# Optimization experiments

Hardware: AMD Instinct MI355X
Metric: run time of the kernel (lower is better)

## Reference

```python
import jax, jax.numpy as jnp
import numpy as np

N_AGT, N_CTX, E, D = 100000, 150000, 500000, 128
EPS = 1e-5


def gn(x, g, b):
    # GroupNorm(1, C) on [N, C] == per-row layernorm over channels
    mu = jnp.mean(x, axis=-1, keepdims=True)
    var = jnp.mean((x - mu) ** 2, axis=-1, keepdims=True)
    return (x - mu) * jax.lax.rsqrt(var + EPS) * g + b


def setup_inputs() -> dict:
    key = jax.random.key(0)
    ks = jax.random.split(key, 24)
    def w(k, i, o):
        return jax.random.normal(k, (i, o), jnp.float32) * (1.0 / np.sqrt(i))
    inp = {
        "agts": jax.random.normal(ks[0], (N_AGT, D), jnp.float32),
        "ctx": jax.random.normal(ks[1], (N_CTX, D), jnp.float32),
        "agt_ctrs": jax.random.normal(ks[2], (N_AGT, 2), jnp.float32),
        "ctx_ctrs": jax.random.normal(ks[3], (N_CTX, 2), jnp.float32),
        # dist MLP: Linear(2,128,bias) -> ReLU -> Linear(128,128,no bias) -> GN -> ReLU
        "W_dist1": w(ks[4], 2, D), "b_dist1": jnp.zeros((D,), jnp.float32),
        "W_dist2": w(ks[5], D, D), "g_dist": jnp.ones((D,), jnp.float32), "b_dist": jnp.zeros((D,), jnp.float32),
        # query: Linear(128,128,no bias) -> GN -> ReLU
        "W_q": w(ks[6], D, D), "g_q": jnp.ones((D,), jnp.float32), "b_q": jnp.zeros((D,), jnp.float32),
        # ctx MLP: Linear(384,128,no bias)->GN->ReLU -> Linear(128,128,no bias)
        "W_c1": w(ks[7], 3 * D, D), "g_c1": jnp.ones((D,), jnp.float32), "b_c1": jnp.zeros((D,), jnp.float32),
        "W_c2": w(ks[8], D, D),
        # agt: Linear(128,128,no bias)
        "W_agt": w(ks[9], D, D),
        # norm after scatter
        "g_n": jnp.ones((D,), jnp.float32), "b_n": jnp.zeros((D,), jnp.float32),
        # linear: Linear(128,128,no bias)->GN (no act)
        "W_lin": w(ks[10], D, D), "g_lin": jnp.ones((D,), jnp.float32), "b_lin": jnp.zeros((D,), jnp.float32),
        # precomputed edge lists (dist<=100 mask in the original)
        "hi": jax.random.randint(ks[11], (E,), 0, N_AGT, jnp.int32),
        "wi": jax.random.randint(ks[12], (E,), 0, N_CTX, jnp.int32),
    }
    return inp


def reference(agts, ctx, agt_ctrs, ctx_ctrs,
              W_dist1, b_dist1, W_dist2, g_dist, b_dist,
              W_q, g_q, b_q,
              W_c1, g_c1, b_c1, W_c2,
              W_agt, g_n, b_n,
              W_lin, g_lin, b_lin,
              hi, wi):
    res = agts
    # gather + dist MLP
    d = agt_ctrs[hi] - ctx_ctrs[wi]                    # [E, 2]
    d = jax.nn.relu(d @ W_dist1 + b_dist1)             # [E, D]
    d = jax.nn.relu(gn(d @ W_dist2, g_dist, b_dist))
    # query from gathered agent features
    q = jax.nn.relu(gn(agts[hi] @ W_q, g_q, b_q))      # [E, D]
    # context message MLP
    c = jnp.concatenate([d, q, ctx[wi]], axis=1)       # [E, 3D]
    c = jax.nn.relu(gn(c @ W_c1, g_c1, b_c1))
    c = c @ W_c2                                       # [E, D]
    # scatter back, norm, residual
    a = agts @ W_agt                                   # [N_agt, D]
    a = a.at[hi].add(c)
    a = jax.nn.relu(gn(a, g_n, b_n))
    a = gn(a @ W_lin, g_lin, b_lin)
    a = jax.nn.relu(a + res)
    return a
```

## Files before the change

kernel.cpp:

```cpp
#include <hip/hip_runtime.h>
#include <math.h>

#define DD 128
#define CAP 32
constexpr float EPS = 1e-5f;

typedef __bf16 bf16x8 __attribute__((ext_vector_type(8)));
typedef float  f32x4  __attribute__((ext_vector_type(4)));

__device__ __forceinline__ float4 ld4(const float* p){ return *(const float4*)p; }

__device__ __forceinline__ bf16x8 cvt8(const float* p){
  bf16x8 r;
#pragma unroll
  for (int i=0;i<8;i++) r[i] = (__bf16)p[i];
  return r;
}

__global__ __launch_bounds__(256)
void pack_w(const float* W0, const float* W1, const float* W2, const float* W3,
            const float* W4, const float* W5, const float* W6, const float* W7,
            __bf16* dst){
  int gidx = blockIdx.x*256 + threadIdx.x;
  int mat  = gidx >> 11;
  int i    = gidx & 2047;
  int lane = i & 63, frag = i >> 6;
  int tn = frag >> 2, ks = frag & 3;
  int n  = tn*16 + (lane & 15);
  int k0 = ks*32 + (lane >> 4)*8;
  const float* W;
  switch(mat){
    case 0: W=W0; break; case 1: W=W1; break; case 2: W=W2; break; case 3: W=W3; break;
    case 4: W=W4; break; case 5: W=W5; break; case 6: W=W6; break; default: W=W7; break;
  }
  __bf16* d = dst + (size_t)mat*16384 + (size_t)i*8;
#pragma unroll
  for (int j=0;j<8;j++) d[j] = (__bf16)W[(size_t)(k0+j)*DD + n];
}

template<bool RELU>
__device__ __forceinline__ void gn_frag(f32x4 (&acc)[8], const float* __restrict__ g,
                                        const float* __restrict__ b, int m){
  float gv[8], bv[8];
#pragma unroll
  for (int t=0;t<8;t++){ gv[t]=g[t*16+m]; bv[t]=b[t*16+m]; }
#pragma unroll
  for (int r=0;r<4;r++){
    float s=0.f, sq=0.f;
#pragma unroll
    for (int t=0;t<8;t++){ float v=acc[t][r]; s+=v; sq=fmaf(v,v,sq); }
#pragma unroll
    for (int mk=1; mk<16; mk<<=1){ s+=__shfl_xor(s,mk,64); sq+=__shfl_xor(sq,mk,64); }
    float mu=s*(1.f/DD);
    float rs=rsqrtf(sq*(1.f/DD)-mu*mu+EPS);
#pragma unroll
    for (int t=0;t<8;t++){
      float v=(acc[t][r]-mu)*rs*gv[t]+bv[t];
      if (RELU) v=fmaxf(v,0.f);
      acc[t][r]=v;
    }
  }
}

__device__ __forceinline__ void mfma_lds(const bf16x8 (&af)[4], const __bf16* WL,
                                         f32x4 (&acc)[8], int lane){
#pragma unroll
  for (int tn=0;tn<8;tn++){
    f32x4 a; a[0]=0.f; a[1]=0.f; a[2]=0.f; a[3]=0.f;
#pragma unroll
    for (int ks=0;ks<4;ks++){
      bf16x8 bf = *(const bf16x8*)(WL + ((tn*4+ks)*64 + lane)*8);
      a = __builtin_amdgcn_mfma_f32_16x16x32_bf16(af[ks], bf, a, 0,0,0);
    }
    acc[tn]=a;
  }
}

__device__ __forceinline__ void stage_w(const __bf16* __restrict__ Wg, __bf16* WL, int w, int lane){
#pragma unroll
  for (int j=0;j<8;j++){
    int off = ((w*8+j)<<10) + lane*16;
    __builtin_amdgcn_global_load_lds(
      (const __attribute__((address_space(1))) void*)((const char*)Wg + off),
      (__attribute__((address_space(3))) void*)((char*)WL + ((w*8+j)<<10)),
      16, 0, 0);
  }
}

__device__ __forceinline__ void read_af(const __bf16* T, bf16x8 (&af)[4], int w, int lane){
  int m=lane&15, q=lane>>4;
#pragma unroll
  for (int ks=0;ks<4;ks++)
    af[ks] = *(const bf16x8*)(T + (16*w+m)*136 + ks*32 + q*8);
}

__device__ __forceinline__ void write_cfrag_bf16(__bf16* T, const f32x4 (&acc)[8], int w, int lane){
  int m=lane&15, q=lane>>4;
#pragma unroll
  for (int r=0;r<4;r++){
    int row=16*w+4*q+r;
#pragma unroll
    for (int t=0;t<8;t++) T[row*136 + t*16 + m] = (__bf16)acc[t][r];
  }
}

__device__ __forceinline__ void load_af_f32(const float* X, bf16x8 (&af)[4], int row, int M, int q){
  if (row < M){
    const float* xr = X + (size_t)row*DD;
#pragma unroll
    for (int ks=0;ks<4;ks++){
      float t[8];
      *(float4*)t     = ld4(xr + ks*32 + q*8);
      *(float4*)(t+4) = ld4(xr + ks*32 + q*8 + 4);
      af[ks] = cvt8(t);
    }
  } else {
#pragma unroll
    for (int ks=0;ks<4;ks++){
#pragma unroll
      for (int j=0;j<8;j++) af[ks][j]=(__bf16)0.f;
    }
  }
}

__global__ __launch_bounds__(256)
void prep_kernel(const int* __restrict__ hi, int E, int* __restrict__ counts, int* __restrict__ perm,
                 const float* __restrict__ agts,
                 const __bf16* __restrict__ Wp_q, const float* __restrict__ g_q, const float* __restrict__ b_q,
                 const __bf16* __restrict__ Wp_mid, const __bf16* __restrict__ Wp_agt,
                 __bf16* __restrict__ Aq2bf, float* __restrict__ baseF, int nA,
                 const float* __restrict__ ctx, const __bf16* __restrict__ Wp_chi,
                 __bf16* __restrict__ Ccbf, int nC,
                 int gBucket, int gA){
  __shared__ __bf16 T[64*136];
  __shared__ __bf16 WL[16384];
  int b = blockIdx.x;
  if (b < gBucket){
    int e = b*256 + threadIdx.x;
    if (e < E){
      int a = hi[e];
      int slot = atomicAdd(&counts[a], 1);
      if (slot < CAP) perm[(size_t)a*CAP + slot] = e;
    }
    return;
  }
  b -= gBucket;
  int tid=threadIdx.x, w=tid>>6, lane=tid&63, m=lane&15, q=lane>>4;
  if (b < gA){
    stage_w(Wp_q, WL, w, lane);
    int rowA = b*64 + 16*w + m;
    bf16x8 af_a[4];
    load_af_f32(agts, af_a, rowA, nA, q);
    f32x4 acc[8];
    __syncthreads();
    mfma_lds(af_a, WL, acc, lane);
    __syncthreads();
    stage_w(Wp_mid, WL, w, lane);
    gn_frag<true>(acc, g_q, b_q, m);
    write_cfrag_bf16(T, acc, w, lane);
    bf16x8 af_q[4];
    read_af(T, af_q, w, lane);
    __syncthreads();
    mfma_lds(af_q, WL, acc, lane);
#pragma unroll
    for (int r=0;r<4;r++){
      int row = b*64 + 16*w + 4*q + r;
      if (row < nA){
#pragma unroll
        for (int t=0;t<8;t++)
          Aq2bf[(size_t)row*DD + t*16 + m] = (__bf16)acc[t][r];
      }
    }
    if (baseF){
      __syncthreads();
      stage_w(Wp_agt, WL, w, lane);
      __syncthreads();
      mfma_lds(af_a, WL, acc, lane);
#pragma unroll
      for (int r=0;r<4;r++){
        int row = b*64 + 16*w + 4*q + r;
        if (row < nA){
#pragma unroll
          for (int t=0;t<8;t++)
            baseF[(size_t)row*DD + t*16 + m] = acc[t][r];
        }
      }
    }
  } else {
    int bid = b - gA;
    stage_w(Wp_chi, WL, w, lane);
    int rowA = bid*64 + 16*w + m;
    bf16x8 af[4];
    load_af_f32(ctx, af, rowA, nC, q);
    f32x4 acc[8];
    __syncthreads();
    mfma_lds(af, WL, acc, lane);
#pragma unroll
    for (int r=0;r<4;r++){
      int row = bid*64 + 16*w + 4*q + r;
      if (row < nC){
#pragma unroll
        for (int t=0;t<8;t++)
          Ccbf[(size_t)row*DD + t*16 + m] = (__bf16)acc[t][r];
      }
    }
  }
}

__global__ __launch_bounds__(256)
void edge_kernel(const float* __restrict__ agt_ctrs, const float* __restrict__ ctx_ctrs,
                 const int* __restrict__ hi, const int* __restrict__ wi,
                 const float* __restrict__ W1, const float* __restrict__ B1,
                 const __bf16* __restrict__ Wp_d2, const float* __restrict__ g_dist, const float* __restrict__ b_dist,
                 const __bf16* __restrict__ Wp_c1, const float* __restrict__ g_c1, const float* __restrict__ b_c1,
                 const __bf16* __restrict__ Wp_c2,
                 const __bf16* __restrict__ Aq2, const __bf16* __restrict__ Cc,
                 float* __restrict__ accOut, __bf16* __restrict__ edge_out, int E){
  __shared__ __bf16 T[64*136];
  __shared__ __bf16 WL[16384];
  int tid=threadIdx.x, w=tid>>6, lane=tid&63, m=lane&15, q=lane>>4;
  int eBase = blockIdx.x*64;
  int grow = tid>>2, gch = tid&3;
  int ge = eBase + grow;
  int ghe=0, gwe=0;
  if (ge < E){ ghe = hi[ge]; gwe = wi[ge]; }
  bf16x8 ga[4], gc[4];
  {
    const __bf16* ap = Aq2 + (size_t)ghe*DD + gch*32;
    const __bf16* cp = Cc  + (size_t)gwe*DD + gch*32;
#pragma unroll
    for (int c2=0;c2<4;c2++){ ga[c2]=*(const bf16x8*)(ap+c2*8); gc[c2]=*(const bf16x8*)(cp+c2*8); }
  }
  stage_w(Wp_d2, WL, w, lane);
  {
    int e0 = lane, e = eBase + e0;
    float dx=0.f, dy=0.f;
    if (e < E){
      int h0=hi[e], w0=wi[e];
      dx = agt_ctrs[2*h0]   - ctx_ctrs[2*w0];
      dy = agt_ctrs[2*h0+1] - ctx_ctrs[2*w0+1];
    }
#pragma unroll
    for (int s=0;s<4;s++){
      float t[8];
#pragma unroll
      for (int j=0;j<8;j++){
        int c = w*32 + s*8 + j;
        t[j] = fmaxf(fmaf(dx, W1[c], fmaf(dy, W1[DD+c], B1[c])), 0.f);
      }
      *(bf16x8*)(T + e0*136 + w*32 + s*8) = cvt8(t);
    }
  }
  __syncthreads();
  bf16x8 af[4]; f32x4 acc[8];
  read_af(T, af, w, lane);
  mfma_lds(af, WL, acc, lane);
  __syncthreads();
  stage_w(Wp_c1, WL, w, lane);
  gn_frag<true>(acc, g_dist, b_dist, m);
  write_cfrag_bf16(T, acc, w, lane);
  read_af(T, af, w, lane);
#pragma unroll
  for (int c2=0;c2<4;c2++){
    float s[8];
#pragma unroll
    for (int j=0;j<8;j++) s[j] = (float)ga[c2][j] + (float)gc[c2][j];
    *(bf16x8*)(T + grow*136 + gch*32 + c2*8) = cvt8(s);
  }
  __syncthreads();
  mfma_lds(af, WL, acc, lane);
#pragma unroll
  for (int r=0;r<4;r++){
    int row = 16*w + 4*q + r;
#pragma unroll
    for (int t=0;t<8;t++)
      acc[t][r] += (float)T[row*136 + t*16 + m];
  }
  __syncthreads();
  stage_w(Wp_c2, WL, w, lane);
  gn_frag<true>(acc, g_c1, b_c1, m);
  write_cfrag_bf16(T, acc, w, lane);
  read_af(T, af, w, lane);
  __syncthreads();
  mfma_lds(af, WL, acc, lane);
  if (edge_out){
    write_cfrag_bf16(T, acc, w, lane);
    if (ge < E){
      const __bf16* src = T + grow*136 + gch*32;
      __bf16* dst = edge_out + (size_t)ge*DD + gch*32;
#pragma unroll
      for (int c2=0;c2<4;c2++) *(bf16x8*)(dst + c2*8) = *(const bf16x8*)(src + c2*8);
    }
  } else {
#pragma unroll
    for (int r=0;r<4;r++){
      int row = 16*w + 4*q + r;
      if (eBase + row < E){
        int he = hi[eBase + row];
        float* dst = accOut + (size_t)he*DD + m;
#pragma unroll
        for (int t=0;t<8;t++)
          atomicAdd(dst + t*16, acc[t][r]);
      }
    }
  }
}

__global__ __launch_bounds__(256)
void final_fused(const float* __restrict__ agts, const __bf16* __restrict__ Wp_agt,
                 const int* __restrict__ counts, const int* __restrict__ perm,
                 const __bf16* __restrict__ edge_out,
                 const float* __restrict__ g_n, const float* __restrict__ b_n,
                 const __bf16* __restrict__ Wp_lin, const float* __restrict__ g_lin, const float* __restrict__ b_lin,
                 float* __restrict__ out, int M){
  __shared__ float Tf[64*132];
  __shared__ __bf16 T[64*136];
  __bf16* WA = (__bf16*)Tf;
  int tid=threadIdx.x, w=tid>>6, lane=tid&63, m=lane&15, q=lane>>4;
  int rowBase=blockIdx.x*64;
  stage_w(Wp_agt, WA, w, lane);
  bf16x8 af_a[4];
  load_af_f32(agts, af_a, rowBase + 16*w + m, M, q);
  f32x4 acc[8];
  __syncthreads();
  mfma_lds(af_a, WA, acc, lane);
  __syncthreads();
#pragma unroll
  for (int r=0;r<4;r++){
    int row=16*w+4*q+r;
#pragma unroll
    for (int t=0;t<8;t++) Tf[row*132 + t*16 + m] = acc[t][r];
  }
  int grow=tid>>2, gch=tid&3;
  int a = rowBase + grow;
  float s[32];
#pragma unroll
  for (int c2=0;c2<8;c2++){
    float4 v = *(const float4*)(Tf + grow*132 + gch*32 + c2*4);
    s[c2*4]=v.x; s[c2*4+1]=v.y; s[c2*4+2]=v.z; s[c2*4+3]=v.w;
  }
  __syncthreads();
  stage_w(Wp_lin, WA, w, lane);
  int cnt = 0;
  if (a < M){ cnt = counts[a]; cnt = cnt < CAP ? cnt : CAP; }
  for (int j=0;j<cnt;j++){
    int e = perm[(size_t)a*CAP + j];
    const __bf16* ep = edge_out + (size_t)e*DD + gch*32;
#pragma unroll
    for (int c2=0;c2<4;c2++){
      bf16x8 v = *(const bf16x8*)(ep + c2*8);
#pragma unroll
      for (int k=0;k<8;k++) s[c2*8+k] += (float)v[k];
    }
  }
  {
    float sm=0.f, sq=0.f;
#pragma unroll
    for (int k=0;k<32;k++){ sm+=s[k]; sq=fmaf(s[k],s[k],sq); }
    sm+=__shfl_xor(sm,1,64); sm+=__shfl_xor(sm,2,64);
    sq+=__shfl_xor(sq,1,64); sq+=__shfl_xor(sq,2,64);
    float mu=sm*(1.f/DD), rs=rsqrtf(sq*(1.f/DD)-mu*mu+EPS);
#pragma unroll
    for (int k=0;k<32;k++){
      int c=gch*32+k;
      s[k]=fmaxf((s[k]-mu)*rs*g_n[c]+b_n[c],0.f);
    }
  }
#pragma unroll
  for (int c2=0;c2<4;c2++)
    *(bf16x8*)(T + grow*136 + gch*32 + c2*8) = cvt8(s + c2*8);
  __syncthreads();
  bf16x8 af[4];
  read_af(T, af, w, lane);
  mfma_lds(af, WA, acc, lane);
  gn_frag<false>(acc, g_lin, b_lin, m);
#pragma unroll
  for (int r=0;r<4;r++){
    int row=rowBase+16*w+4*q+r;
    if (row<M){
#pragma unroll
      for (int t=0;t<8;t++){
        int col=t*16+m;
        float rr=agts[(size_t)row*DD+col];
        out[(size_t)row*DD+col]=fmaxf(acc[t][r]+rr,0.f);
      }
    }
  }
}

__global__ __launch_bounds__(256)
void final_kernel(const float* __restrict__ accF, const float* __restrict__ g_n, const float* __restrict__ b_n,
                  const __bf16* __restrict__ Wp_lin, const float* __restrict__ g_lin, const float* __restrict__ b_lin,
                  const float* __restrict__ res, float* __restrict__ out, int M){
  __shared__ __bf16 Ab[64*136];
  __shared__ __bf16 WL[16384];
  int tid=threadIdx.x, w=tid>>6, lane=tid&63, m=lane&15, q=lane>>4;
  int rowBase=blockIdx.x*64;
  stage_w(Wp_lin, WL, w, lane);
  {
    int rl=tid>>2, qq=tid&3;
    int row=rowBase+rl;
    float v[32];
    float s=0.f, sq=0.f;
#pragma unroll
    for (int t8=0;t8<8;t8++){
      float4 x=make_float4(0.f,0.f,0.f,0.f);
      if (row<M) x=ld4(accF + (size_t)row*DD + qq*32 + t8*4);
      v[t8*4]=x.x; v[t8*4+1]=x.y; v[t8*4+2]=x.z; v[t8*4+3]=x.w;
      s  += x.x+x.y+x.z+x.w;
      sq += x.x*x.x+x.y*x.y+x.z*x.z+x.w*x.w;
    }
    s+=__shfl_xor(s,1,64); s+=__shfl_xor(s,2,64);
    sq+=__shfl_xor(sq,1,64); sq+=__shfl_xor(sq,2,64);
    float mu=s*(1.f/DD), rs=rsqrtf(sq*(1.f/DD)-mu*mu+EPS);
#pragma unroll
    for (int j=0;j<32;j++){
      int c=qq*32+j;
      v[j]=fmaxf((v[j]-mu)*rs*g_n[c]+b_n[c],0.f);
    }
#pragma unroll
    for (int s2=0;s2<4;s2++)
      *(bf16x8*)(Ab + rl*136 + qq*32 + s2*8) = cvt8(v+s2*8);
  }
  __syncthreads();
  bf16x8 af[4]; f32x4 acc[8];
  read_af(Ab, af, w, lane);
  mfma_lds(af, WL, acc, lane);
  gn_frag<false>(acc, g_lin, b_lin, m);
#pragma unroll
  for (int r=0;r<4;r++){
    int row=rowBase+16*w+4*q+r;
    if (row<M){
#pragma unroll
      for (int t=0;t<8;t++){
        int col=t*16+m;
        float rr=res[(size_t)row*DD+col];
        out[(size_t)row*DD+col]=fmaxf(acc[t][r]+rr,0.f);
      }
    }
  }
}

extern "C" void kernel_launch(void* const* d_in, const int* in_sizes, int n_in,
                              void* d_out, int out_size, void* d_ws, size_t ws_size,
                              hipStream_t stream){
  const float* agts     = (const float*)d_in[0];
  const float* ctx      = (const float*)d_in[1];
  const float* agt_ctrs = (const float*)d_in[2];
  const float* ctx_ctrs = (const float*)d_in[3];
  const float* W_dist1  = (const float*)d_in[4];
  const float* b_dist1  = (const float*)d_in[5];
  const float* W_dist2  = (const float*)d_in[6];
  const float* g_dist   = (const float*)d_in[7];
  const float* b_dist   = (const float*)d_in[8];
  const float* W_q      = (const float*)d_in[9];
  const float* g_q      = (const float*)d_in[10];
  const float* b_q      = (const float*)d_in[11];
  const float* W_c1     = (const float*)d_in[12];
  const float* g_c1     = (const float*)d_in[13];
  const float* b_c1     = (const float*)d_in[14];
  const float* W_c2     = (const float*)d_in[15];
  const float* W_agt    = (const float*)d_in[16];
  const float* g_n      = (const float*)d_in[17];
  const float* b_n      = (const float*)d_in[18];
  const float* W_lin    = (const float*)d_in[19];
  const float* g_lin    = (const float*)d_in[20];
  const float* b_lin    = (const float*)d_in[21];
  const int*   hi       = (const int*)d_in[22];
  const int*   wi       = (const int*)d_in[23];

  int nA = in_sizes[0]/DD, nC = in_sizes[1]/DD, nE = in_sizes[22];
  float* out = (float*)d_out;

  auto al = [](size_t x){ return (x + 255) & ~(size_t)255; };
  size_t oAq2 = 0;
  size_t oCc  = al(oAq2 + (size_t)nA*DD*2);
  size_t oWp  = al(oCc  + (size_t)nC*DD*2);
  size_t oCnt = al(oWp  + (size_t)8*16384*2);
  size_t oPerm= al(oCnt + (size_t)nA*4);
  size_t oTail= al(oPerm+ (size_t)nA*CAP*4);
  size_t needA = oTail + (size_t)nE*DD*2;
  bool bigA = (ws_size >= needA);

  char* ws = (char*)d_ws;
  __bf16* Aq2bf = (__bf16*)(ws + oAq2);
  __bf16* Ccbf  = (__bf16*)(ws + oCc);
  __bf16* Wp    = (__bf16*)(ws + oWp);
  int*    counts= (int*)   (ws + oCnt);
  int*    perm  = (int*)   (ws + oPerm);
  __bf16* edge_out = (__bf16*)(ws + oTail);
  float*  CF    = (float*)(ws + oCnt);

  dim3 B(256);
  int gA=(nA+63)/64, gC=(nC+63)/64, gE=(nE+63)/64;
  int gBucket = bigA ? (nE+255)/256 : 0;

  pack_w<<<64,B,0,stream>>>(W_dist2, W_c1, W_c2, W_q,
                            W_c1+128*DD, W_c1+256*DD, W_agt, W_lin, Wp);
  if (bigA){
    hipMemsetAsync(counts, 0, (size_t)nA*4, stream);
    prep_kernel<<<gBucket+gA+gC,B,0,stream>>>(hi, nE, counts, perm,
        agts, Wp+3*16384, g_q, b_q, Wp+4*16384, Wp+6*16384, Aq2bf, nullptr, nA,
        ctx, Wp+5*16384, Ccbf, nC, gBucket, gA);
    edge_kernel<<<gE,B,0,stream>>>(agt_ctrs, ctx_ctrs, hi, wi,
        W_dist1, b_dist1, Wp+0, g_dist, b_dist,
        Wp+1*16384, g_c1, b_c1, Wp+2*16384,
        Aq2bf, Ccbf, nullptr, edge_out, nE);
    final_fused<<<gA,B,0,stream>>>(agts, Wp+6*16384, counts, perm, edge_out,
        g_n, b_n, Wp+7*16384, g_lin, b_lin, out, nA);
  } else {
    prep_kernel<<<gA+gC,B,0,stream>>>(hi, nE, counts, perm,
        agts, Wp+3*16384, g_q, b_q, Wp+4*16384, Wp+6*16384, Aq2bf, CF, nA,
        ctx, Wp+5*16384, Ccbf, nC, 0, gA);
    edge_kernel<<<gE,B,0,stream>>>(agt_ctrs, ctx_ctrs, hi, wi,
        W_dist1, b_dist1, Wp+0, g_dist, b_dist,
        Wp+1*16384, g_c1, b_c1, Wp+2*16384,
        Aq2bf, Ccbf, CF, nullptr, nE);
    final_kernel<<<gA,B,0,stream>>>(CF, g_n, b_n, Wp+7*16384, g_lin, b_lin, agts, out, nA);
  }
}
```

Measured before the change: 487.6 us.

## Process 128 edges per edge_kernel block with 512 threads sharing staged weights

The edge kernel tile grows from 64 to 128 edges per block, using 8 waves instead of 4. Each staged 32KB weight matrix in LDS is now reused by twice as many rows, and each wave loads only half the weight chunks through a new stage_w8 helper. The distance-MLP prologue is remapped so the 8 waves cover 128 rows by 4 column groups. The cost is 16KB more LDS per block and fewer, larger blocks, which can lower occupancy or scheduling flexibility.

```diff
diff --git a/kernel.cpp b/kernel.cpp
--- a/kernel.cpp
+++ b/kernel.cpp
@@ -83,6 +83,18 @@
     __builtin_amdgcn_global_load_lds(
       (const __attribute__((address_space(1))) void*)((const char*)Wg + off),
       (__attribute__((address_space(3))) void*)((char*)WL + ((w*8+j)<<10)),
+      16, 0, 0);
+  }
+}
+
+__device__ __forceinline__ void stage_w8(const __bf16* __restrict__ Wg, __bf16* WL, int w, int lane){
+#pragma unroll
+  for (int j=0;j<4;j++){
+    int c = j*8 + w;
+    int off = (c<<10) + lane*16;
+    __builtin_amdgcn_global_load_lds(
+      (const __attribute__((address_space(1))) void*)((const char*)Wg + off),
+      (__attribute__((address_space(3))) void*)((char*)WL + (c<<10)),
       16, 0, 0);
   }
 }
@@ -207,7 +219,7 @@
   }
 }
 
-__global__ __launch_bounds__(256)
+__global__ __launch_bounds__(512)
 void edge_kernel(const float* __restrict__ agt_ctrs, const float* __restrict__ ctx_ctrs,
                  const int* __restrict__ hi, const int* __restrict__ wi,
                  const float* __restrict__ W1, const float* __restrict__ B1,
@@ -216,10 +228,10 @@
                  const __bf16* __restrict__ Wp_c2,
                  const __bf16* __restrict__ Aq2, const __bf16* __restrict__ Cc,
                  float* __restrict__ accOut, __bf16* __restrict__ edge_out, int E){
-  __shared__ __bf16 T[64*136];
+  __shared__ __bf16 T[128*136];
   __shared__ __bf16 WL[16384];
   int tid=threadIdx.x, w=tid>>6, lane=tid&63, m=lane&15, q=lane>>4;
-  int eBase = blockIdx.x*64;
+  int eBase = blockIdx.x*128;
   int grow = tid>>2, gch = tid&3;
   int ge = eBase + grow;
   int ghe=0, gwe=0;
@@ -231,9 +243,11 @@
 #pragma unroll
     for (int c2=0;c2<4;c2++){ ga[c2]=*(const bf16x8*)(ap+c2*8); gc[c2]=*(const bf16x8*)(cp+c2*8); }
   }
-  stage_w(Wp_d2, WL, w, lane);
+  stage_w8(Wp_d2, WL, w, lane);
   {
-    int e0 = lane, e = eBase + e0;
+    int e0 = ((w>>2)<<6) + lane;
+    int wc = (w&3)*32;
+    int e = eBase + e0;
     float dx=0.f, dy=0.f;
     if (e < E){
       int h0=hi[e], w0=wi[e];
@@ -245,10 +259,10 @@
       float t[8];
 #pragma unroll
       for (int j=0;j<8;j++){
-        int c = w*32 + s*8 + j;
+        int c = wc + s*8 + j;
         t[j] = fmaxf(fmaf(dx, W1[c], fmaf(dy, W1[DD+c], B1[c])), 0.f);
       }
-      *(bf16x8*)(T + e0*136 + w*32 + s*8) = cvt8(t);
+      *(bf16x8*)(T + e0*136 + wc + s*8) = cvt8(t);
     }
   }
   __syncthreads();
@@ -256,7 +270,7 @@
   read_af(T, af, w, lane);
   mfma_lds(af, WL, acc, lane);
   __syncthreads();
-  stage_w(Wp_c1, WL, w, lane);
+  stage_w8(Wp_c1, WL, w, lane);
   gn_frag<true>(acc, g_dist, b_dist, m);
   write_cfrag_bf16(T, acc, w, lane);
   read_af(T, af, w, lane);
@@ -277,7 +291,7 @@
       acc[t][r] += (float)T[row*136 + t*16 + m];
   }
   __syncthreads();
-  stage_w(Wp_c2, WL, w, lane);
+  stage_w8(Wp_c2, WL, w, lane);
   gn_frag<true>(acc, g_c1, b_c1, m);
   write_cfrag_bf16(T, acc, w, lane);
   read_af(T, af, w, lane);
@@ -491,8 +505,8 @@
   __bf16* edge_out = (__bf16*)(ws + oTail);
   float*  CF    = (float*)(ws + oCnt);
 
-  dim3 B(256);
-  int gA=(nA+63)/64, gC=(nC+63)/64, gE=(nE+63)/64;
+  dim3 B(256), B2(512);
+  int gA=(nA+63)/64, gC=(nC+63)/64, gE=(nE+127)/128;
   int gBucket = bigA ? (nE+255)/256 : 0;
 
   pack_w<<<64,B,0,stream>>>(W_dist2, W_c1, W_c2, W_q,
@@ -502,7 +516,7 @@
     prep_kernel<<<gBucket+gA+gC,B,0,stream>>>(hi, nE, counts, perm,
         agts, Wp+3*16384, g_q, b_q, Wp+4*16384, Wp+6*16384, Aq2bf, nullptr, nA,
         ctx, Wp+5*16384, Ccbf, nC, gBucket, gA);
-    edge_kernel<<<gE,B,0,stream>>>(agt_ctrs, ctx_ctrs, hi, wi,
+    edge_kernel<<<gE,B2,0,stream>>>(agt_ctrs, ctx_ctrs, hi, wi,
         W_dist1, b_dist1, Wp+0, g_dist, b_dist,
         Wp+1*16384, g_c1, b_c1, Wp+2*16384,
         Aq2bf, Ccbf, nullptr, edge_out, nE);
@@ -512,7 +526,7 @@
     prep_kernel<<<gA+gC,B,0,stream>>>(hi, nE, counts, perm,
         agts, Wp+3*16384, g_q, b_q, Wp+4*16384, Wp+6*16384, Aq2bf, CF, nA,
         ctx, Wp+5*16384, Ccbf, nC, 0, gA);
-    edge_kernel<<<gE,B,0,stream>>>(agt_ctrs, ctx_ctrs, hi, wi,
+    edge_kernel<<<gE,B2,0,stream>>>(agt_ctrs, ctx_ctrs, hi, wi,
         W_dist1, b_dist1, Wp+0, g_dist, b_dist,
         Wp+1*16384, g_c1, b_c1, Wp+2*16384,
         Aq2bf, Ccbf, CF, nullptr, nE);
```

New measurement: 479.0 us. Within noise of the previous version (-1.8%).

## Process 128 edges per block with two M-tiles per wave in edge kernel

Applied to the files above, without the earlier changes.

The edge kernel now handles 128 edges per block instead of 64. Each wave computes two 16-row MFMA tiles that share each B-fragment read from LDS, which halves weight-staging traffic per edge and cuts LDS reads of weights per MFMA. The cost is a doubled T buffer in LDS and twice the accumulator registers. A launch-bounds hint of 2 blocks per SM is added to limit register growth, with a risk of spills or lower occupancy.

```diff
diff --git a/kernel.cpp b/kernel.cpp
--- a/kernel.cpp
+++ b/kernel.cpp
@@ -76,6 +76,23 @@
   }
 }
 
+__device__ __forceinline__ void mfma_lds2(const bf16x8 (&af0)[4], const bf16x8 (&af1)[4],
+                                          const __bf16* WL,
+                                          f32x4 (&acc0)[8], f32x4 (&acc1)[8], int lane){
+#pragma unroll
+  for (int tn=0;tn<8;tn++){
+    f32x4 a0; a0[0]=0.f; a0[1]=0.f; a0[2]=0.f; a0[3]=0.f;
+    f32x4 a1; a1[0]=0.f; a1[1]=0.f; a1[2]=0.f; a1[3]=0.f;
+#pragma unroll
+    for (int ks=0;ks<4;ks++){
+      bf16x8 bf = *(const bf16x8*)(WL + ((tn*4+ks)*64 + lane)*8);
+      a0 = __builtin_amdgcn_mfma_f32_16x16x32_bf16(af0[ks], bf, a0, 0,0,0);
+      a1 = __builtin_amdgcn_mfma_f32_16x16x32_bf16(af1[ks], bf, a1, 0,0,0);
+    }
+    acc0[tn]=a0; acc1[tn]=a1;
+  }
+}
+
 __device__ __forceinline__ void stage_w(const __bf16* __restrict__ Wg, __bf16* WL, int w, int lane){
 #pragma unroll
   for (int j=0;j<8;j++){
@@ -94,6 +111,16 @@
     af[ks] = *(const bf16x8*)(T + (16*w+m)*136 + ks*32 + q*8);
 }
 
+__device__ __forceinline__ void read_af2(const __bf16* T, bf16x8 (&af0)[4], bf16x8 (&af1)[4],
+                                         int rb, int lane){
+  int m=lane&15, q=lane>>4;
+#pragma unroll
+  for (int ks=0;ks<4;ks++){
+    af0[ks] = *(const bf16x8*)(T + (rb+m)*136    + ks*32 + q*8);
+    af1[ks] = *(const bf16x8*)(T + (rb+16+m)*136 + ks*32 + q*8);
+  }
+}
+
 __device__ __forceinline__ void write_cfrag_bf16(__bf16* T, const f32x4 (&acc)[8], int w, int lane){
   int m=lane&15, q=lane>>4;
 #pragma unroll
@@ -101,6 +128,20 @@
     int row=16*w+4*q+r;
 #pragma unroll
     for (int t=0;t<8;t++) T[row*136 + t*16 + m] = (__bf16)acc[t][r];
+  }
+}
+
+__device__ __forceinline__ void write_cfrag2(__bf16* T, const f32x4 (&acc0)[8], const f32x4 (&acc1)[8],
+                                             int rb, int lane){
+  int m=lane&15, q=lane>>4;
+#pragma unroll
+  for (int r=0;r<4;r++){
+    int row0=rb+4*q+r, row1=rb+16+4*q+r;
+#pragma unroll
+    for (int t=0;t<8;t++){
+      T[row0*136 + t*16 + m] = (__bf16)acc0[t][r];
+      T[row1*136 + t*16 + m] = (__bf16)acc1[t][r];
+    }
   }
 }
 
@@ -207,7 +248,7 @@
   }
 }
 
-__global__ __launch_bounds__(256)
+__global__ __launch_bounds__(256,2)
 void edge_kernel(const float* __restrict__ agt_ctrs, const float* __restrict__ ctx_ctrs,
                  const int* __restrict__ hi, const int* __restrict__ wi,
                  const float* __restrict__ W1, const float* __restrict__ B1,
@@ -216,24 +257,26 @@
                  const __bf16* __restrict__ Wp_c2,
                  const __bf16* __restrict__ Aq2, const __bf16* __restrict__ Cc,
                  float* __restrict__ accOut, __bf16* __restrict__ edge_out, int E){
-  __shared__ __bf16 T[64*136];
+  __shared__ __bf16 T[128*136];
   __shared__ __bf16 WL[16384];
   int tid=threadIdx.x, w=tid>>6, lane=tid&63, m=lane&15, q=lane>>4;
-  int eBase = blockIdx.x*64;
-  int grow = tid>>2, gch = tid&3;
+  int eBase = blockIdx.x*128;
+  int rb = 32*w;
+  int grow = tid>>1, gch = tid&1;
   int ge = eBase + grow;
   int ghe=0, gwe=0;
   if (ge < E){ ghe = hi[ge]; gwe = wi[ge]; }
-  bf16x8 ga[4], gc[4];
+  bf16x8 ga[8], gc[8];
   {
-    const __bf16* ap = Aq2 + (size_t)ghe*DD + gch*32;
-    const __bf16* cp = Cc  + (size_t)gwe*DD + gch*32;
-#pragma unroll
-    for (int c2=0;c2<4;c2++){ ga[c2]=*(const bf16x8*)(ap+c2*8); gc[c2]=*(const bf16x8*)(cp+c2*8); }
+    const __bf16* ap = Aq2 + (size_t)ghe*DD + gch*64;
+    const __bf16* cp = Cc  + (size_t)gwe*DD + gch*64;
+#pragma unroll
+    for (int c2=0;c2<8;c2++){ ga[c2]=*(const bf16x8*)(ap+c2*8); gc[c2]=*(const bf16x8*)(cp+c2*8); }
   }
   stage_w(Wp_d2, WL, w, lane);
   {
-    int e0 = lane, e = eBase + e0;
+    int e0 = grow, wc = gch*64;
+    int e = eBase + e0;
     float dx=0.f, dy=0.f;
     if (e < E){
       int h0=hi[e], w0=wi[e];
@@ -241,66 +284,75 @@
       dy = agt_ctrs[2*h0+1] - ctx_ctrs[2*w0+1];
     }
 #pragma unroll
-    for (int s=0;s<4;s++){
+    for (int s=0;s<8;s++){
       float t[8];
 #pragma unroll
       for (int j=0;j<8;j++){
-        int c = w*32 + s*8 + j;
+        int c = wc + s*8 + j;
         t[j] = fmaxf(fmaf(dx, W1[c], fmaf(dy, W1[DD+c], B1[c])), 0.f);
       }
-      *(bf16x8*)(T + e0*136 + w*32 + s*8) = cvt8(t);
-    }
-  }
-  __syncthreads();
-  bf16x8 af[4]; f32x4 acc[8];
-  read_af(T, af, w, lane);
-  mfma_lds(af, WL, acc, lane);
+      *(bf16x8*)(T + e0*136 + wc + s*8) = cvt8(t);
+    }
+  }
+  __syncthreads();
+  bf16x8 af0[4], af1[4]; f32x4 acc0[8], acc1[8];
+  read_af2(T, af0, af1, rb, lane);
+  mfma_lds2(af0, af1, WL, acc0, acc1, lane);
   __syncthreads();
   stage_w(Wp_c1, WL, w, lane);
-  gn_frag<true>(acc, g_dist, b_dist, m);
-  write_cfrag_bf16(T, acc, w, lane);
-  read_af(T, af, w, lane);
-#pragma unroll
-  for (int c2=0;c2<4;c2++){
+  gn_frag<true>(acc0, g_dist, b_dist, m);
+  gn_frag<true>(acc1, g_dist, b_dist, m);
+  write_cfrag2(T, acc0, acc1, rb, lane);
+  read_af2(T, af0, af1, rb, lane);
+#pragma unroll
+  for (int c2=0;c2<8;c2++){
     float s[8];
 #pragma unroll
     for (int j=0;j<8;j++) s[j] = (float)ga[c2][j] + (float)gc[c2][j];
-    *(bf16x8*)(T + grow*136 + gch*32 + c2*8) = cvt8(s);
-  }
-  __syncthreads();
-  mfma_lds(af, WL, acc, lane);
-#pragma unroll
-  for (int r=0;r<4;r++){
-    int row = 16*w + 4*q + r;
-#pragma unroll
-    for (int t=0;t<8;t++)
-      acc[t][r] += (float)T[row*136 + t*16 + m];
+    *(bf16x8*)(T + grow*136 + gch*64 + c2*8) = cvt8(s);
+  }
+  __syncthreads();
+  mfma_lds2(af0, af1, WL, acc0, acc1, lane);
+#pragma unroll
+  for (int r=0;r<4;r++){
+    int row0 = rb + 4*q + r, row1 = rb + 16 + 4*q + r;
+#pragma unroll
+    for (int t=0;t<8;t++){
+      acc0[t][r] += (float)T[row0*136 + t*16 + m];
+      acc1[t][r] += (float)T[row1*136 + t*16 + m];
+    }
   }
   __syncthreads();
   stage_w(Wp_c2, WL, w, lane);
-  gn_frag<true>(acc, g_c1, b_c1, m);
-  write_cfrag_bf16(T, acc, w, lane);
-  read_af(T, af, w, lane);
-  __syncthreads();
-  mfma_lds(af, WL, acc, lane);
+  gn_frag<true>(acc0, g_c1, b_c1, m);
+  gn_frag<true>(acc1, g_c1, b_c1, m);
+  write_cfrag2(T, acc0, acc1, rb, lane);
+  read_af2(T, af0, af1, rb, lane);
+  __syncthreads();
+  mfma_lds2(af0, af1, WL, acc0, acc1, lane);
   if (edge_out){
-    write_cfrag_bf16(T, acc, w, lane);
+    write_cfrag2(T, acc0, acc1, rb, lane);
     if (ge < E){
-      const __bf16* src = T + grow*136 + gch*32;
-      __bf16* dst = edge_out + (size_t)ge*DD + gch*32;
-#pragma unroll
-      for (int c2=0;c2<4;c2++) *(bf16x8*)(dst + c2*8) = *(const bf16x8*)(src + c2*8);
+      const __bf16* src = T + grow*136 + gch*64;
+      __bf16* dst = edge_out + (size_t)ge*DD + gch*64;
+#pragma unroll
+      for (int c2=0;c2<8;c2++) *(bf16x8*)(dst + c2*8) = *(const bf16x8*)(src + c2*8);
     }
   } else {
 #pragma unroll
     for (int r=0;r<4;r++){
-      int row = 16*w + 4*q + r;
-      if (eBase + row < E){
-        int he = hi[eBase + row];
+      int row0 = rb + 4*q + r, row1 = rb + 16 + 4*q + r;
+      if (eBase + row0 < E){
+        int he = hi[eBase + row0];
         float* dst = accOut + (size_t)he*DD + m;
 #pragma unroll
-        for (int t=0;t<8;t++)
-          atomicAdd(dst + t*16, acc[t][r]);
+        for (int t=0;t<8;t++) atomicAdd(dst + t*16, acc0[t][r]);
+      }
+      if (eBase + row1 < E){
+        int he = hi[eBase + row1];
+        float* dst = accOut + (size_t)he*DD + m;
+#pragma unroll
+        for (int t=0;t<8;t++) atomicAdd(dst + t*16, acc1[t][r]);
       }
     }
   }
@@ -492,7 +544,7 @@
   float*  CF    = (float*)(ws + oCnt);
 
   dim3 B(256);
-  int gA=(nA+63)/64, gC=(nC+63)/64, gE=(nE+63)/64;
+  int gA=(nA+63)/64, gC=(nC+63)/64, gE=(nE+127)/128;
   int gBucket = bigA ? (nE+255)/256 : 0;
 
   pack_w<<<64,B,0,stream>>>(W_dist2, W_c1, W_c2, W_q,
```

After: 511.0 us. 4.8% more time.
